# Kernel tuning notes

Hardware: AMD Instinct MI355X
Metric: run time of the kernel (lower is better)

The kernel has to match this reference:

```python
import jax, jax.numpy as jnp
import numpy as np

DIM = 64
LSH_NUM_PROJS = 7
BLOCK_SIZE = 256
SAMPLE_SIZE = 256
MIN_SEQ_LEN = 2048


def _unit_hamming(n):
    # Gray-code-like permutation used by AngularLSH so adjacent hash ids differ by 1 bit
    a = np.arange(2)
    for i in range(1, n):
        a = np.concatenate([a, a[::-1] + 2 ** i])
    return jnp.asarray(a, dtype=jnp.int32)

_PERM = _unit_hamming(LSH_NUM_PROJS)                                  # [2^P]
_ENC = (2 ** jnp.arange(LSH_NUM_PROJS)).reshape(1, 1, 1, LSH_NUM_PROJS)


def _lsh_hash(mat, proj_dir):
    # mat: [b,h,n,d], proj_dir: [1,1,d,P] -> hash ids [b,h,n]
    mask = jnp.matmul(mat, proj_dir) > 0
    bin_ids = (mask * _ENC).sum(-1)
    return _PERM[bin_ids]


def _exact_attention(q, k, v, scale, causal=False, bias=None):
    qk = jnp.einsum('bhnd,bhmd->bhnm', q, k) * scale
    if causal:
        n, m = q.shape[2], k.shape[2]
        qk = qk + jnp.triu(jnp.full((n, m), jnp.finfo(q.dtype).min, q.dtype), 1)[None, None]
    if bias is not None:
        qk = qk + bias
    lse = jax.scipy.special.logsumexp(qk, axis=-1, keepdims=True)      # [b,h,n,1]
    out = jnp.einsum('bhnm,bhmd->bhnd', jnp.exp(qk - lse), v)
    return out, lse


def _add_attn(a1, l1, a2, l2):
    c = (1.0 / (1.0 + jnp.exp(l2 - l1))).astype(a1.dtype)
    attn = c * a1 + (1 - c) * a2
    lse = l1 - jnp.log(c + jnp.finfo(l1.dtype).eps)
    return attn, lse


def _indexing(x, idx, chunk_size=-1):
    # x: [b,h,n,d], idx: [b,h,s] -> [b,h,s,d] (padded up to a multiple of chunk_size)
    g = jnp.take_along_axis(x, idx[..., None], axis=2)
    n = g.shape[2]
    if chunk_size > 0 and n % chunk_size != 0:
        pad = -n % chunk_size
        g = jnp.pad(g, ((0, 0), (0, 0), (0, pad), (0, 0)))
    return g


def _no_causal(q, k, v, scale, proj_dir, level):
    b, h, n_q, d = q.shape
    n_k = k.shape[2]
    if MIN_SEQ_LEN > n_q:
        return _exact_attention(q, k, v, scale, causal=False)
    q_idx = jnp.argsort(_lsh_hash(q, proj_dir), axis=2)
    k_idx = jnp.argsort(_lsh_hash(k, proj_dir), axis=2)
    q_idx_inv = jnp.argsort(q_idx, axis=2)
    kbs = BLOCK_SIZE
    q_s = _indexing(q, q_idx, kbs)
    k_s = _indexing(k, k_idx, kbs)
    v_s = _indexing(v, k_idx, kbs)
    num_blocks = k_s.shape[2] // kbs
    qbs = q_s.shape[2] // num_blocks
    # block-diagonal attention over LSH-sorted buckets
    q_blk = q_s.reshape(-1, 1, qbs, d)
    k_blk = k_s.reshape(-1, 1, kbs, d)
    v_blk = v_s.reshape(-1, 1, kbs, d)
    attn_block, lse_block = _exact_attention(q_blk, k_blk, v_blk, scale, causal=False)
    attn_block = attn_block.reshape(b, h, q_s.shape[2], -1)
    lse_block = lse_block.reshape(b, h, q_s.shape[2], -1)
    if q_s.shape[2] != n_q:
        attn_block = attn_block[:, :, :n_q, :]
        lse_block = lse_block[:, :, :n_q, :]
        q_s = q_s[:, :, :n_q, :]
        k_s = k_s[:, :, :n_k, :]
        v_s = v_s[:, :, :n_k, :]
    S = SAMPLE_SIZE
    if S > 0 and n_q > qbs and n_k > kbs:
        rng = jax.random.fold_in(jax.random.key(42), level)
        sampled = jax.random.randint(rng, (b, h, S), 0, n_k)
        v_sub = _indexing(v_s, sampled)
        k_sub = _indexing(k_s, sampled)
        offset = jnp.arange(n_q)[None, :, None]                         # (1,n,1)
        bm = (offset // qbs) == (sampled // kbs).reshape(-1, 1, S)      # (b*h,n,S)
        bias = bm.reshape(b, h, n_q, S).astype(q_s.dtype) * jnp.finfo(q_s.dtype).min
        attn_res, lse_res = _exact_attention(q_s, k_sub, v_sub, scale, causal=False, bias=bias)
        lse_res = lse_res + jnp.asarray(np.log(n_k / S), lse_res.dtype)
        attn, lse = _add_attn(attn_block, lse_block, attn_res, lse_res)
    else:
        attn, lse = attn_block, lse_block
    attn = _indexing(attn, q_idx_inv)
    lse = _indexing(lse, q_idx_inv)
    return attn, lse


def _hyper(q, k, v, scale, proj_dir, level=0):
    b, h, n_k, d = k.shape
    n_q = q.shape[2]
    if n_k <= MIN_SEQ_LEN:
        return _exact_attention(q, k, v, scale, causal=True)
    # recursive causal split: block-diagonal halves + un-masked lower-left quadrant
    q_bd = q.reshape(b, 2 * h, n_q // 2, d)
    k_bd = k.reshape(b, 2 * h, n_k // 2, d)
    v_bd = v.reshape(b, 2 * h, n_k // 2, d)
    attn_bd, lse_bd = _hyper(q_bd, k_bd, v_bd, scale, proj_dir, level + 1)
    attn_bd = attn_bd.reshape(b, h, -1, d)
    lse_bd = lse_bd.reshape(b, h, -1, 1)
    a_un, l_un = _no_causal(q[:, :, n_k // 2:, :], k[:, :, :n_k // 2, :],
                            v[:, :, :n_k // 2, :], scale, proj_dir, 100 + level)
    a_up, l_up = attn_bd[:, :, :n_q // 2, :], lse_bd[:, :, :n_q // 2, :]
    a_dn, l_dn = _add_attn(attn_bd[:, :, n_q // 2:, :], lse_bd[:, :, n_q // 2:, :], a_un, l_un)
    return jnp.concatenate([a_up, a_dn], axis=2), jnp.concatenate([l_up, l_dn], axis=2)


def setup_inputs() -> dict:
    rng = jax.random.key(0)
    kq, kk, kv, kp = jax.random.split(rng, 4)
    B, H, N, D = 1, 8, 8192, 64
    return {
        'query': jax.random.normal(kq, (B, H, N, D), jnp.float32),
        'key': jax.random.normal(kk, (B, H, N, D), jnp.float32),
        'value': jax.random.normal(kv, (B, H, N, D), jnp.float32),
        'proj_dir': jax.random.normal(kp, (1, 1, D, LSH_NUM_PROJS), jnp.float32),
    }


def reference(query, key, value, proj_dir):
    scale = query.shape[-1] ** -0.5
    attn, lse = _hyper(query, key, value, scale, proj_dir)
    return attn
```

## Files before the change

### kernel.cpp

```cpp
#include <hip/hip_runtime.h>
#include <stdint.h>
#include <math.h>

#define H 8
#define NSEQ 8192
#define D 64
#define SC2 0.18033688011112042f
#define LN2F 0.69314718055994531f
#define THR2 10.0f
#define EPSF 1.1920928955078125e-07f

typedef short v8s __attribute__((ext_vector_type(8)));
typedef float v4f __attribute__((ext_vector_type(4)));
typedef unsigned short ushort_t;

#define MFMA16(a,b,c) __builtin_amdgcn_mfma_f32_16x16x32_bf16((a),(b),(c),0,0,0)
#define SWZ(row, cb)    (((row)*128) + ((cb) ^ ((((row)&7))<<4)))
#define SWZ256(row, cb) (((row)*256) + ((cb) ^ ((((row)&7))<<4)))

__device__ __forceinline__ float exp2x(float x){
  float r; asm("v_exp_f32 %0, %1" : "=v"(r) : "v"(x)); return r;
}
__device__ __forceinline__ unsigned int cvtpk(float a, float b){
  unsigned int r; asm("v_cvt_pk_bf16_f32 %0, %1, %2" : "=v"(r) : "v"(a), "v"(b)); return r;
}
#define VONES (v8s){0x3F80,0x3F80,0x3F80,0x3F80,0x3F80,0x3F80,0x3F80,0x3F80}

__global__ __launch_bounds__(256) void prep_hash(
    const float* __restrict__ q, const float* __restrict__ k, const float* __restrict__ v,
    const float* __restrict__ proj,
    ushort_t* __restrict__ qb, ushort_t* __restrict__ kb, ushort_t* __restrict__ vb,
    int* __restrict__ hq, int* __restrict__ hk)
{
  __shared__ float tile[64][65];
  __shared__ float pj[448];
  __shared__ int pbuf[4][64];
  const int bid = blockIdx.x;
  const int t = threadIdx.x;
  if (bid >= 2048){
    const int tix = bid - 2048;
    size_t off = (size_t)tix*4096 + t*16;
    float4 f0 = *(const float4*)(v + off);
    float4 f1 = *(const float4*)(v + off + 4);
    float4 f2 = *(const float4*)(v + off + 8);
    float4 f3 = *(const float4*)(v + off + 12);
    uint4 o0, o1;
    o0.x = cvtpk(f0.x, f0.y);  o0.y = cvtpk(f0.z, f0.w);
    o0.z = cvtpk(f1.x, f1.y);  o0.w = cvtpk(f1.z, f1.w);
    o1.x = cvtpk(f2.x, f2.y);  o1.y = cvtpk(f2.z, f2.w);
    o1.z = cvtpk(f3.x, f3.y);  o1.w = cvtpk(f3.z, f3.w);
    *(uint4*)(vb + off) = o0;
    *(uint4*)(vb + off + 8) = o1;
    return;
  }
  const int isk = bid & 1;
  const int tix = bid >> 1;
  const int rowbase = tix << 6;
  const float* src = isk ? k : q;
  ushort_t* dstb = isk ? kb : qb;
  int* dsth = isk ? hk : hq;
  for (int i = t; i < 448; i += 256) pj[i] = proj[i];
  {
    const int r = t >> 2, cg = (t & 3) << 4;
    const float* s = src + (size_t)(rowbase + r)*64 + cg;
    float4 f0 = *(const float4*)(s);
    float4 f1 = *(const float4*)(s + 4);
    float4 f2 = *(const float4*)(s + 8);
    float4 f3 = *(const float4*)(s + 12);
    tile[r][cg+0]=f0.x;  tile[r][cg+1]=f0.y;  tile[r][cg+2]=f0.z;  tile[r][cg+3]=f0.w;
    tile[r][cg+4]=f1.x;  tile[r][cg+5]=f1.y;  tile[r][cg+6]=f1.z;  tile[r][cg+7]=f1.w;
    tile[r][cg+8]=f2.x;  tile[r][cg+9]=f2.y;  tile[r][cg+10]=f2.z; tile[r][cg+11]=f2.w;
    tile[r][cg+12]=f3.x; tile[r][cg+13]=f3.y; tile[r][cg+14]=f3.z; tile[r][cg+15]=f3.w;
    uint4 o0, o1;
    o0.x = cvtpk(f0.x, f0.y);  o0.y = cvtpk(f0.z, f0.w);
    o0.z = cvtpk(f1.x, f1.y);  o0.w = cvtpk(f1.z, f1.w);
    o1.x = cvtpk(f2.x, f2.y);  o1.y = cvtpk(f2.z, f2.w);
    o1.z = cvtpk(f3.x, f3.y);  o1.w = cvtpk(f3.z, f3.w);
    *(uint4*)(dstb + (size_t)(rowbase + r)*64 + cg) = o0;
    *(uint4*)(dstb + (size_t)(rowbase + r)*64 + cg + 8) = o1;
  }
  __syncthreads();
  {
    const int r = t & 63, pg = t >> 6;
    const int p2 = (pg < 3) ? (pg + 4) : 6;
    float d0 = 0.0f, d1 = 0.0f;
    for (int d = 0; d < 64; ++d){
      float x = tile[r][d];
      d0 = fmaf(x, pj[d*7 + pg], d0);
      d1 = fmaf(x, pj[d*7 + p2], d1);
    }
    int pb = (d0 > 0.0f ? (1 << pg) : 0);
    if (pg < 3 && d1 > 0.0f) pb |= (1 << (pg + 4));
    pbuf[pg][r] = pb;
  }
  __syncthreads();
  if (t < 64){
    int b = pbuf[0][t] | pbuf[1][t] | pbuf[2][t] | pbuf[3][t];
    dsth[rowbase + t] = b ^ (b >> 1);
  }
}

__device__ __forceinline__ void tf2x32(uint32_t k0, uint32_t k1,
                                       uint32_t x0, uint32_t x1,
                                       uint32_t& o0, uint32_t& o1)
{
  uint32_t ks0 = k0, ks1 = k1, ks2 = k0 ^ k1 ^ 0x1BD11BDAu;
  x0 += ks0; x1 += ks1;
#define RND(r) { x0 += x1; x1 = (x1 << (r)) | (x1 >> (32-(r))); x1 ^= x0; }
  RND(13) RND(15) RND(26) RND(6)  x0 += ks1; x1 += ks2 + 1u;
  RND(17) RND(29) RND(16) RND(24) x0 += ks2; x1 += ks0 + 2u;
  RND(13) RND(15) RND(26) RND(6)  x0 += ks0; x1 += ks1 + 3u;
  RND(17) RND(29) RND(16) RND(24) x0 += ks1; x1 += ks2 + 4u;
  RND(13) RND(15) RND(26) RND(6)  x0 += ks2; x1 += ks0 + 5u;
#undef RND
  o0 = x0; o1 = x1;
}

__device__ __forceinline__ void qk8(const v8s qf[2], const char* Ks, int lo, int hi, v4f sa[8]){
  __builtin_amdgcn_s_setprio(1);
#pragma unroll
  for (int st = 0; st < 8; ++st){
#pragma unroll
    for (int kc = 0; kc < 2; ++kc){
      v8s bf = *(const v8s*)(Ks + SWZ(st*16 + lo, kc*64 + hi*16));
      sa[st] = MFMA16(qf[kc], bf, sa[st]);
    }
  }
  __builtin_amdgcn_s_setprio(0);
}

__device__ __forceinline__ void sm_pv8(v4f sa[8], char* Pw, const char* VTs,
                                       int lo, int hi, float m[4], v4f o[5]){
  float tm[4];
  bool grow = false;
#pragma unroll
  for (int reg = 0; reg < 4; ++reg){
    float a = fmaxf(fmaxf(sa[0][reg], sa[1][reg]), fmaxf(sa[2][reg], sa[3][reg]));
    float b = fmaxf(fmaxf(sa[4][reg], sa[5][reg]), fmaxf(sa[6][reg], sa[7][reg]));
    tm[reg] = fmaxf(a, b);
    grow = grow || (tm[reg] > m[reg] + THR2);
  }
  if (__any(grow)){
#pragma unroll
    for (int reg = 0; reg < 4; ++reg){
      float t = tm[reg];
      t = fmaxf(t, __shfl_xor(t, 1));
      t = fmaxf(t, __shfl_xor(t, 2));
      t = fmaxf(t, __shfl_xor(t, 4));
      t = fmaxf(t, __shfl_xor(t, 8));
      float mn = fmaxf(m[reg], t);
      float corr = exp2x(m[reg] - mn);
      m[reg] = mn;
#pragma unroll
      for (int dt = 0; dt < 5; ++dt) o[dt][reg] *= corr;
    }
  }
#pragma unroll
  for (int reg = 0; reg < 4; ++reg){
    float mr = m[reg];
    uint4 pw;
    pw.x = cvtpk(exp2x(sa[0][reg]-mr), exp2x(sa[1][reg]-mr));
    pw.y = cvtpk(exp2x(sa[2][reg]-mr), exp2x(sa[3][reg]-mr));
    pw.z = cvtpk(exp2x(sa[4][reg]-mr), exp2x(sa[5][reg]-mr));
    pw.w = cvtpk(exp2x(sa[6][reg]-mr), exp2x(sa[7][reg]-mr));
    *(uint4*)(Pw + SWZ256(hi*4 + reg, 16*lo)) = pw;
  }
  asm volatile("" ::: "memory");
  __builtin_amdgcn_s_setprio(1);
#pragma unroll
  for (int kb = 0; kb < 4; ++kb){
    v8s pa = *(const v8s*)(Pw + SWZ256(lo, kb*64 + hi*16));
#pragma unroll
    for (int dt = 0; dt < 4; ++dt){
      v8s vbr = *(const v8s*)(VTs + SWZ256(dt*16 + lo, kb*64 + hi*16));
      o[dt] = MFMA16(pa, vbr, o[dt]);
    }
    o[4] = MFMA16(pa, VONES, o[4]);
  }
  __builtin_amdgcn_s_setprio(0);
}

__device__ __forceinline__ void vt_write(char* VTs, uint2 vr0, uint2 vr1, uint2 vr2, uint2 vr3,
                                         int vdg, int vlo, int vsth){
  const int cb = 16*vlo + vsth*8;
  uint2 w;
  w.x = (vr0.x & 0xFFFFu) | ((vr1.x & 0xFFFFu) << 16);
  w.y = (vr2.x & 0xFFFFu) | ((vr3.x & 0xFFFFu) << 16);
  *(uint2*)(VTs + SWZ256(vdg*4 + 0, cb)) = w;
  w.x = (vr0.x >> 16) | (vr1.x & 0xFFFF0000u);
  w.y = (vr2.x >> 16) | (vr3.x & 0xFFFF0000u);
  *(uint2*)(VTs + SWZ256(vdg*4 + 1, cb)) = w;
  w.x = (vr0.y & 0xFFFFu) | ((vr1.y & 0xFFFFu) << 16);
  w.y = (vr2.y & 0xFFFFu) | ((vr3.y & 0xFFFFu) << 16);
  *(uint2*)(VTs + SWZ256(vdg*4 + 2, cb)) = w;
  w.x = (vr0.y >> 16) | (vr1.y & 0xFFFF0000u);
  w.y = (vr2.y >> 16) | (vr3.y & 0xFFFF0000u);
  *(uint2*)(VTs + SWZ256(vdg*4 + 3, cb)) = w;
}

__global__ __launch_bounds__(512, 4) void diag_sort(
    const ushort_t* __restrict__ qb, const ushort_t* __restrict__ kb, const ushort_t* __restrict__ vb,
    float* __restrict__ out, float* __restrict__ lse,
    const int* __restrict__ hq, const int* __restrict__ hk,
    int* __restrict__ q100, int* __restrict__ k100,
    int* __restrict__ q101, int* __restrict__ k101,
    int* __restrict__ s100, int* __restrict__ s101)
{
  __shared__ __align__(16) char lds[66048];
  const int bid0 = blockIdx.x;
  const int tid = threadIdx.x;

  if (bid0 < 48){
    unsigned short (*hist)[128] = (unsigned short(*)[128])lds;
    unsigned short (*off )[128] = (unsigned short(*)[128])(lds + 32768);
    int* bstart = (int*)(lds + 65536);
    const int t = tid;
    if (t < 128){
      int gid = bid0*128 + t;
      int level, span, idx; int* outp;
      if (gid < 2048){ level = 100; span = 4096; outp = s100; idx = gid; }
      else           { level = 101; span = 2048; outp = s101; idx = gid - 2048; }
      uint32_t r0, r1; tf2x32(0u, 42u, 0u, (uint32_t)level, r0, r1);
      uint32_t k20, k21; tf2x32(r0, r1, 0u, 1u, k20, k21);
      uint32_t o0, o1; tf2x32(k20, k21, 0u, (uint32_t)idx, o0, o1);
      outp[idx] = (int)((o0 ^ o1) % (uint32_t)span);
    }
    const int* src = nullptr; int n = 0, base = 0; int* outp = nullptr;
    if (bid0 < 8)       { int h = bid0;     src = hq + h*NSEQ + 4096;        n = 4096; base = 4096;          outp = q100 + h*4096; }
    else if (bid0 < 16) { int h = bid0 - 8; src = hk + h*NSEQ;               n = 4096; base = 0;             outp = k100 + h*4096; }
    else if (bid0 < 32) { int id = bid0-16; int h = id>>1, p = id&1;
                          src = hq + h*NSEQ + p*4096 + 2048;                 n = 2048; base = p*4096 + 2048; outp = q101 + id*2048; }
    else                { int id = bid0-32; int h = id>>1, p = id&1;
                          src = hk + h*NSEQ + p*4096;                        n = 2048; base = p*4096;       outp = k101 + id*2048; }
    const int chunk = n >> 7;
    if (t < 128) for (int b = 0; b < 128; ++b) hist[t][b] = 0;
    __syncthreads();
    const int* mysrc = src + (t & 127) * chunk;
    if (t < 128) for (int i = 0; i < chunk; ++i) hist[t][mysrc[i]]++;
    __syncthreads();
    if (t < 128){
      int s = 0;
      for (int tt = 0; tt < 128; ++tt) s += hist[tt][t];
      bstart[t] = s;
    }
    __syncthreads();
    if (t == 0){
      int run = 0;
      for (int b = 0; b < 128; ++b){ int c = bstart[b]; bstart[b] = run; run += c; }
    }
    __syncthreads();
    if (t < 128){
      unsigned int run = (unsigned int)bstart[t];
      for (int tt = 0; tt < 128; ++tt){ off[tt][t] = (unsigned short)run; run += hist[tt][t]; }
    }
    __syncthreads();
    if (t < 128){
      for (int i = 0; i < chunk; ++i){
        int hsh = mysrc[i];
        unsigned short pos = off[t][hsh]++;
        outp[pos] = base + t * chunk + i;
      }
    }
    return;
  }

  char* Ks  = lds;
  char* VTs = lds + 16384;
  char* Ps  = lds + 32768;
  const int bid = bid0 - 48;
  const int xcd = bid & 7, sl = bid >> 3;
  const int inst = xcd*4 + (sl >> 4);
  const int pi = sl & 15;
  const int h = inst >> 2, tblk = inst & 3;
  const size_t hoff = (size_t)h * NSEQ * D;
  const ushort_t* qh = qb + hoff; const ushort_t* kh = kb + hoff; const ushort_t* vh = vb + hoff;
  const int blkbase = tblk * 2048;
  const int w = tid >> 6, lane = tid & 63;
  const int lo = lane & 15, hi = lane >> 4;
  char* Pw = Ps + w*4096;
  const int kr = tid >> 2, kq = tid & 3;
  const int vlo = tid & 15, vdg = (tid >> 4) & 15, vsth = tid >> 8;

  const int qt  = (w < 4) ? (31 - pi) : pi;
  const int wq  = w & 3;
  const int nkt   = (31 - pi)/2 + 1;
  const int mynkt = qt/2 + 1;
  const int qpos0 = qt*64 + wq*16;

  v8s qf[2];
  {
    const ushort_t* r = qh + (size_t)(blkbase + qpos0 + lo) * D;
    qf[0] = *(const v8s*)(r + hi*8);
    qf[1] = *(const v8s*)(r + 32 + hi*8);
  }
  const v4f vz = {0.0f, 0.0f, 0.0f, 0.0f};
  v4f o[5] = {vz, vz, vz, vz, vz};
  float m[4] = {-INFINITY, -INFINITY, -INFINITY, -INFINITY};

  uint4 kreg0, kreg1; uint2 vr0, vr1, vr2, vr3;
#define DLOAD(kt) { \
    const ushort_t* ksr = kh + (size_t)(blkbase + (kt)*128 + kr)*D + kq*16; \
    kreg0 = *(const uint4*)ksr; \
    kreg1 = *(const uint4*)(ksr + 8); \
    const ushort_t* vs = vh + (size_t)(blkbase + (kt)*128 + vsth*64 + vlo)*D + vdg*4; \
    vr0 = *(const uint2*)(vs); \
    vr1 = *(const uint2*)(vs + 16*D); \
    vr2 = *(const uint2*)(vs + 32*D); \
    vr3 = *(const uint2*)(vs + 48*D); }

  DLOAD(0);
#pragma unroll 1
  for (int kt = 0; kt < nkt; ++kt){
    *(uint4*)(Ks + SWZ(kr, kq*32))      = kreg0;
    *(uint4*)(Ks + SWZ(kr, kq*32 + 16)) = kreg1;
    vt_write(VTs, vr0, vr1, vr2, vr3, vdg, vlo, vsth);
    __syncthreads();
    if (kt + 1 < nkt) DLOAD(kt+1);
    if (kt < mynkt){
      v4f sa[8] = {vz, vz, vz, vz, vz, vz, vz, vz};
      qk8(qf, Ks, lo, hi, sa);
#pragma unroll
      for (int st = 0; st < 8; ++st) sa[st] *= SC2;
      if (kt == mynkt - 1){
#pragma unroll
        for (int st = 0; st < 8; ++st){
          int kpos = kt*128 + st*16 + lo;
#pragma unroll
          for (int reg = 0; reg < 4; ++reg)
            if (kpos > qpos0 + hi*4 + reg) sa[st][reg] = -INFINITY;
        }
      }
      sm_pv8(sa, Pw, VTs, lo, hi, m, o);
    }
    __syncthreads();
  }
#undef DLOAD
#pragma unroll
  for (int reg = 0; reg < 4; ++reg){
    int rw = blkbase + qpos0 + hi*4 + reg;
    float lsum = o[4][reg];
    float inv = 1.0f / lsum;
#pragma unroll
    for (int dt = 0; dt < 4; ++dt)
      out[hoff + (size_t)rw*D + dt*16 + lo] = o[dt][reg] * inv;
    if (lo == 0) lse[h*NSEQ + rw] = m[reg]*LN2F + logf(lsum);
  }
}

__device__ __forceinline__ int nc_key(const int* __restrict__ ki, const int* __restrict__ sp,
                                      int qblk, int kt, int pos, int& msk){
  if (kt < 2){ msk = 0; return ki[qblk*256 + kt*128 + pos]; }
  int s = sp[(kt-2)*128 + pos]; msk = ((s >> 8) == qblk) ? 1 : 0; return ki[s];
}

template<int LEVEL>
__global__ __launch_bounds__(512, 4) void nc_mfma(
    const ushort_t* __restrict__ qb, const ushort_t* __restrict__ kb, const ushort_t* __restrict__ vb,
    float* __restrict__ out, float* __restrict__ lse,
    const int* __restrict__ qidx, const int* __restrict__ kidx, const int* __restrict__ samp)
{
  __shared__ __align__(16) char Ks[16384];
  __shared__ __align__(16) char VTs[16384];
  __shared__ __align__(16) char Ps[8][4096];
  __shared__ int kmk[128];
  const int bid = blockIdx.x;
  int inst, jb;
  if (LEVEL == 101){ int xcd = bid & 7, sl = bid >> 3; inst = xcd*2 + (sl >> 4); jb = sl & 15; }
  else             { inst = bid & 7; jb = bid >> 3; }
  const float delta2 = (LEVEL == 101) ? 3.0f : 4.0f;
  const int seglen = (LEVEL == 101) ? 2048 : 4096;
  const int* qi = qidx + inst*seglen;
  const int* ki = kidx + inst*seglen;
  const int* sp = samp + inst*256;
  const int h = (LEVEL == 101) ? (inst >> 1) : inst;
  const int qblk = jb >> 1;
  const size_t hoff = (size_t)h * NSEQ * D;
  const ushort_t* qh = qb + hoff; const ushort_t* kh = kb + hoff; const ushort_t* vh = vb + hoff;
  const int tid = threadIdx.x;
  const int w = tid >> 6, lane = tid & 63;
  const int lo = lane & 15, hi = lane >> 4;
  char* Pw = Ps[w];
  const int kr = tid >> 2, kq = tid & 3;
  const int vlo = tid & 15, vdg = (tid >> 4) & 15, vsth = tid >> 8;

  int orig[4];
  v8s qf[2];
  {
    int qrl = qi[jb*128 + w*16 + lo];
    const ushort_t* r = qh + (size_t)qrl * D;
    qf[0] = *(const v8s*)(r + hi*8);
    qf[1] = *(const v8s*)(r + 32 + hi*8);
#pragma unroll
    for (int reg = 0; reg < 4; ++reg) orig[reg] = qi[jb*128 + w*16 + hi*4 + reg];
  }
  const v4f vz = {0.0f, 0.0f, 0.0f, 0.0f};
  v4f o[5] = {vz, vz, vz, vz, vz};
  float m[4] = {-INFINITY, -INFINITY, -INFINITY, -INFINITY};

  uint4 kreg0, kreg1; uint2 vr0, vr1, vr2, vr3; int msk;
#define NLOAD(kt) { \
    int krow = nc_key(ki, sp, qblk, kt, kr, msk); \
    const ushort_t* ksr = kh + (size_t)krow*D + kq*16; \
    kreg0 = *(const uint4*)ksr; \
    kreg1 = *(const uint4*)(ksr + 8); \
    int m_; \
    int g0 = nc_key(ki, sp, qblk, kt, vsth*64 + vlo,      m_); \
    int g1 = nc_key(ki, sp, qblk, kt, vsth*64 + 16 + vlo, m_); \
    int g2 = nc_key(ki, sp, qblk, kt, vsth*64 + 32 + vlo, m_); \
    int g3 = nc_key(ki, sp, qblk, kt, vsth*64 + 48 + vlo, m_); \
    vr0 = *(const uint2*)(vh + (size_t)g0*D + vdg*4); \
    vr1 = *(const uint2*)(vh + (size_t)g1*D + vdg*4); \
    vr2 = *(const uint2*)(vh + (size_t)g2*D + vdg*4); \
    vr3 = *(const uint2*)(vh + (size_t)g3*D + vdg*4); }

  NLOAD(0);
#pragma unroll 1
  for (int kt = 0; kt < 4; ++kt){
    *(uint4*)(Ks + SWZ(kr, kq*32))      = kreg0;
    *(uint4*)(Ks + SWZ(kr, kq*32 + 16)) = kreg1;
    if (kq == 0) kmk[kr] = msk;
    vt_write(VTs, vr0, vr1, vr2, vr3, vdg, vlo, vsth);
    __syncthreads();
    if (kt + 1 < 4) NLOAD(kt+1);
    v4f sa[8] = {vz, vz, vz, vz, vz, vz, vz, vz};
    qk8(qf, Ks, lo, hi, sa);
    if (kt < 2){
#pragma unroll
      for (int st = 0; st < 8; ++st) sa[st] *= SC2;
    } else {
#pragma unroll
      for (int st = 0; st < 8; ++st){
        if (kmk[st*16 + lo]) sa[st] = (v4f){-INFINITY, -INFINITY, -INFINITY, -INFINITY};
        else                 sa[st] = sa[st]*SC2 + delta2;
      }
    }
    sm_pv8(sa, Pw, VTs, lo, hi, m, o);
    __syncthreads();
  }
#undef NLOAD
#pragma unroll
  for (int reg = 0; reg < 4; ++reg){
    int og = orig[reg];
    float lsum = o[4][reg];
    float l1v = lse[h*NSEQ + og];
    float l2v = m[reg]*LN2F + logf(lsum);
    float c = 1.0f / (1.0f + __expf(l2v - l1v));
    float inv = (1.0f - c) / lsum;
#pragma unroll
    for (int dt = 0; dt < 4; ++dt){
      float* ap = out + hoff + (size_t)og*D + dt*16 + lo;
      *ap = c * (*ap) + inv * o[dt][reg];
    }
    if (lo == 0) lse[h*NSEQ + og] = l1v - logf(c + EPSF);
  }
}

extern "C" void kernel_launch(void* const* d_in, const int* in_sizes, int n_in,
                              void* d_out, int out_size, void* d_ws, size_t ws_size,
                              hipStream_t stream)
{
  const float* q    = (const float*)d_in[0];
  const float* k    = (const float*)d_in[1];
  const float* v    = (const float*)d_in[2];
  const float* proj = (const float*)d_in[3];
  float* out = (float*)d_out;

  char* ws = (char*)d_ws;
  float* lse = (float*)ws;
  int* hq   = (int*)(ws + 262144);
  int* hk   = (int*)(ws + 524288);
  int* q100 = (int*)(ws + 786432);
  int* k100 = (int*)(ws + 917504);
  int* q101 = (int*)(ws + 1048576);
  int* k101 = (int*)(ws + 1179648);
  int* s100 = (int*)(ws + 1310720);
  int* s101 = (int*)(ws + 1318912);
  ushort_t* qb = (ushort_t*)(ws + 1335296);
  ushort_t* kb = qb + (size_t)H*NSEQ*D;
  ushort_t* vb = kb + (size_t)H*NSEQ*D;

  prep_hash    <<<dim3(3072), dim3(256), 0, stream>>>(q, k, v, proj, qb, kb, vb, hq, hk);
  diag_sort    <<<dim3(560),  dim3(512), 0, stream>>>(qb, kb, vb, out, lse, hq, hk,
                                                      q100, k100, q101, k101, s100, s101);
  nc_mfma<101> <<<dim3(256),  dim3(512), 0, stream>>>(qb, kb, vb, out, lse, q101, k101, s101);
  nc_mfma<100> <<<dim3(256),  dim3(512), 0, stream>>>(qb, kb, vb, out, lse, q100, k100, s100);
}
```

Before: 113.0 us.

## Run both non-causal levels in one launch and merge level-100 results afterward

The level-101 and level-100 non-causal attention kernels are fused into a single 512-block launch so both can run concurrently instead of back-to-back. Level 100 now writes its normalized partial output as bf16 plus its LSE to a scratch buffer, and a new merge kernel combines that with the existing output. The per-wave P buffer is halved by doing the softmax/PV step in two 128-key halves, and the histogram is narrowed to bytes, cutting LDS use to raise occupancy. The trade-off is an extra kernel launch, an extra round trip through global memory, and bf16 rounding of the level-100 partial result.

```diff
diff --git a/kernel.cpp b/kernel.cpp
--- a/kernel.cpp
+++ b/kernel.cpp
@@ -23,6 +23,11 @@
 }
 __device__ __forceinline__ unsigned int cvtpk(float a, float b){
   unsigned int r; asm("v_cvt_pk_bf16_f32 %0, %1, %2" : "=v"(r) : "v"(a), "v"(b)); return r;
+}
+__device__ __forceinline__ ushort_t f2bf(float f){
+  union { float f; unsigned int u; } c; c.f = f;
+  unsigned int u = c.u + 0x7FFFu + ((c.u >> 16) & 1u);
+  return (ushort_t)(u >> 16);
 }
 #define VONES (v8s){0x3F80,0x3F80,0x3F80,0x3F80,0x3F80,0x3F80,0x3F80,0x3F80}
 
@@ -129,8 +134,8 @@
   __builtin_amdgcn_s_setprio(0);
 }
 
-__device__ __forceinline__ void sm_pv8(v4f sa[8], char* Pw, const char* VTs,
-                                       int lo, int hi, float m[4], v4f o[5]){
+__device__ __forceinline__ void sm_pv8s(v4f sa[8], char* Pw, const char* VTs,
+                                        int lo, int hi, float m[4], v4f o[5]){
   float tm[4];
   bool grow = false;
 #pragma unroll
@@ -156,33 +161,35 @@
     }
   }
 #pragma unroll
-  for (int reg = 0; reg < 4; ++reg){
-    float mr = m[reg];
-    uint4 pw;
-    pw.x = cvtpk(exp2x(sa[0][reg]-mr), exp2x(sa[1][reg]-mr));
-    pw.y = cvtpk(exp2x(sa[2][reg]-mr), exp2x(sa[3][reg]-mr));
-    pw.z = cvtpk(exp2x(sa[4][reg]-mr), exp2x(sa[5][reg]-mr));
-    pw.w = cvtpk(exp2x(sa[6][reg]-mr), exp2x(sa[7][reg]-mr));
-    *(uint4*)(Pw + SWZ256(hi*4 + reg, 16*lo)) = pw;
-  }
-  asm volatile("" ::: "memory");
-  __builtin_amdgcn_s_setprio(1);
-#pragma unroll
-  for (int kb = 0; kb < 4; ++kb){
-    v8s pa = *(const v8s*)(Pw + SWZ256(lo, kb*64 + hi*16));
-#pragma unroll
-    for (int dt = 0; dt < 4; ++dt){
-      v8s vbr = *(const v8s*)(VTs + SWZ256(dt*16 + lo, kb*64 + hi*16));
-      o[dt] = MFMA16(pa, vbr, o[dt]);
-    }
-    o[4] = MFMA16(pa, VONES, o[4]);
-  }
-  __builtin_amdgcn_s_setprio(0);
-}
-
-__device__ __forceinline__ void vt_write(char* VTs, uint2 vr0, uint2 vr1, uint2 vr2, uint2 vr3,
-                                         int vdg, int vlo, int vsth){
-  const int cb = 16*vlo + vsth*8;
+  for (int hh = 0; hh < 2; ++hh){
+#pragma unroll
+    for (int reg = 0; reg < 4; ++reg){
+      float mr = m[reg];
+      uint2 pw;
+      pw.x = cvtpk(exp2x(sa[hh*4+0][reg]-mr), exp2x(sa[hh*4+1][reg]-mr));
+      pw.y = cvtpk(exp2x(sa[hh*4+2][reg]-mr), exp2x(sa[hh*4+3][reg]-mr));
+      *(uint2*)(Pw + SWZ(hi*4 + reg, 8*lo)) = pw;
+    }
+    asm volatile("" ::: "memory");
+    __builtin_amdgcn_s_setprio(1);
+#pragma unroll
+    for (int kb = 0; kb < 2; ++kb){
+      v8s pa = *(const v8s*)(Pw + SWZ(lo, kb*64 + hi*16));
+#pragma unroll
+      for (int dt = 0; dt < 4; ++dt){
+        v8s vbr = *(const v8s*)(VTs + SWZ256(dt*16 + lo, hh*128 + kb*64 + hi*16));
+        o[dt] = MFMA16(pa, vbr, o[dt]);
+      }
+      o[4] = MFMA16(pa, VONES, o[4]);
+    }
+    __builtin_amdgcn_s_setprio(0);
+    asm volatile("" ::: "memory");
+  }
+}
+
+__device__ __forceinline__ void vt_write_h(char* VTs, uint2 vr0, uint2 vr1, uint2 vr2, uint2 vr3,
+                                           int vdg, int vlo, int vsth){
+  const int cb = vsth*128 + vlo*8;
   uint2 w;
   w.x = (vr0.x & 0xFFFFu) | ((vr1.x & 0xFFFFu) << 16);
   w.y = (vr2.x & 0xFFFFu) | ((vr3.x & 0xFFFFu) << 16);
@@ -206,14 +213,14 @@
     int* __restrict__ q101, int* __restrict__ k101,
     int* __restrict__ s100, int* __restrict__ s101)
 {
-  __shared__ __align__(16) char lds[66048];
+  __shared__ __align__(16) char lds[49664];
   const int bid0 = blockIdx.x;
   const int tid = threadIdx.x;
 
   if (bid0 < 48){
-    unsigned short (*hist)[128] = (unsigned short(*)[128])lds;
-    unsigned short (*off )[128] = (unsigned short(*)[128])(lds + 32768);
-    int* bstart = (int*)(lds + 65536);
+    unsigned char  (*hist)[128] = (unsigned char (*)[128])lds;
+    unsigned short (*off )[128] = (unsigned short(*)[128])(lds + 16384);
+    int* bstart = (int*)(lds + 49152);
     const int t = tid;
     if (t < 128){
       int gid = bid0*128 + t;
@@ -277,7 +284,7 @@
   const int blkbase = tblk * 2048;
   const int w = tid >> 6, lane = tid & 63;
   const int lo = lane & 15, hi = lane >> 4;
-  char* Pw = Ps + w*4096;
+  char* Pw = Ps + w*2048;
   const int kr = tid >> 2, kq = tid & 3;
   const int vlo = tid & 15, vdg = (tid >> 4) & 15, vsth = tid >> 8;
 
@@ -313,7 +320,7 @@
   for (int kt = 0; kt < nkt; ++kt){
     *(uint4*)(Ks + SWZ(kr, kq*32))      = kreg0;
     *(uint4*)(Ks + SWZ(kr, kq*32 + 16)) = kreg1;
-    vt_write(VTs, vr0, vr1, vr2, vr3, vdg, vlo, vsth);
+    vt_write_h(VTs, vr0, vr1, vr2, vr3, vdg, vlo, vsth);
     __syncthreads();
     if (kt + 1 < nkt) DLOAD(kt+1);
     if (kt < mynkt){
@@ -330,7 +337,7 @@
             if (kpos > qpos0 + hi*4 + reg) sa[st][reg] = -INFINITY;
         }
       }
-      sm_pv8(sa, Pw, VTs, lo, hi, m, o);
+      sm_pv8s(sa, Pw, VTs, lo, hi, m, o);
     }
     __syncthreads();
   }
@@ -353,26 +360,31 @@
   int s = sp[(kt-2)*128 + pos]; msk = ((s >> 8) == qblk) ? 1 : 0; return ki[s];
 }
 
-template<int LEVEL>
-__global__ __launch_bounds__(512, 4) void nc_mfma(
+__global__ __launch_bounds__(512, 4) void nc_both(
     const ushort_t* __restrict__ qb, const ushort_t* __restrict__ kb, const ushort_t* __restrict__ vb,
     float* __restrict__ out, float* __restrict__ lse,
-    const int* __restrict__ qidx, const int* __restrict__ kidx, const int* __restrict__ samp)
+    const int* __restrict__ q101, const int* __restrict__ k101, const int* __restrict__ s101,
+    const int* __restrict__ q100, const int* __restrict__ k100, const int* __restrict__ s100,
+    ushort_t* __restrict__ a100, float* __restrict__ lse100)
 {
   __shared__ __align__(16) char Ks[16384];
   __shared__ __align__(16) char VTs[16384];
-  __shared__ __align__(16) char Ps[8][4096];
+  __shared__ __align__(16) char Ps[8][2048];
   __shared__ int kmk[128];
   const int bid = blockIdx.x;
-  int inst, jb;
-  if (LEVEL == 101){ int xcd = bid & 7, sl = bid >> 3; inst = xcd*2 + (sl >> 4); jb = sl & 15; }
-  else             { inst = bid & 7; jb = bid >> 3; }
-  const float delta2 = (LEVEL == 101) ? 3.0f : 4.0f;
-  const int seglen = (LEVEL == 101) ? 2048 : 4096;
-  const int* qi = qidx + inst*seglen;
-  const int* ki = kidx + inst*seglen;
-  const int* sp = samp + inst*256;
-  const int h = (LEVEL == 101) ? (inst >> 1) : inst;
+  const bool lvl101 = bid < 256;
+  int inst, jb; float delta2; int seglen;
+  const int *qi, *ki, *sp;
+  if (lvl101){
+    int xcd = bid & 7, sl = bid >> 3; inst = xcd*2 + (sl >> 4); jb = sl & 15;
+    delta2 = 3.0f; seglen = 2048;
+    qi = q101 + inst*seglen; ki = k101 + inst*seglen; sp = s101 + inst*256;
+  } else {
+    int b2 = bid - 256; inst = b2 & 7; jb = b2 >> 3;
+    delta2 = 4.0f; seglen = 4096;
+    qi = q100 + inst*seglen; ki = k100 + inst*seglen; sp = s100 + inst*256;
+  }
+  const int h = lvl101 ? (inst >> 1) : inst;
   const int qblk = jb >> 1;
   const size_t hoff = (size_t)h * NSEQ * D;
   const ushort_t* qh = qb + hoff; const ushort_t* kh = kb + hoff; const ushort_t* vh = vb + hoff;
@@ -419,7 +431,7 @@
     *(uint4*)(Ks + SWZ(kr, kq*32))      = kreg0;
     *(uint4*)(Ks + SWZ(kr, kq*32 + 16)) = kreg1;
     if (kq == 0) kmk[kr] = msk;
-    vt_write(VTs, vr0, vr1, vr2, vr3, vdg, vlo, vsth);
+    vt_write_h(VTs, vr0, vr1, vr2, vr3, vdg, vlo, vsth);
     __syncthreads();
     if (kt + 1 < 4) NLOAD(kt+1);
     v4f sa[8] = {vz, vz, vz, vz, vz, vz, vz, vz};
@@ -434,25 +446,67 @@
         else                 sa[st] = sa[st]*SC2 + delta2;
       }
     }
-    sm_pv8(sa, Pw, VTs, lo, hi, m, o);
+    sm_pv8s(sa, Pw, VTs, lo, hi, m, o);
     __syncthreads();
   }
 #undef NLOAD
-#pragma unroll
-  for (int reg = 0; reg < 4; ++reg){
-    int og = orig[reg];
-    float lsum = o[4][reg];
-    float l1v = lse[h*NSEQ + og];
-    float l2v = m[reg]*LN2F + logf(lsum);
-    float c = 1.0f / (1.0f + __expf(l2v - l1v));
-    float inv = (1.0f - c) / lsum;
-#pragma unroll
-    for (int dt = 0; dt < 4; ++dt){
-      float* ap = out + hoff + (size_t)og*D + dt*16 + lo;
-      *ap = c * (*ap) + inv * o[dt][reg];
-    }
-    if (lo == 0) lse[h*NSEQ + og] = l1v - logf(c + EPSF);
-  }
+  if (lvl101){
+#pragma unroll
+    for (int reg = 0; reg < 4; ++reg){
+      int og = orig[reg];
+      float lsum = o[4][reg];
+      float l1v = lse[h*NSEQ + og];
+      float l2v = m[reg]*LN2F + logf(lsum);
+      float c = 1.0f / (1.0f + __expf(l2v - l1v));
+      float inv = (1.0f - c) / lsum;
+#pragma unroll
+      for (int dt = 0; dt < 4; ++dt){
+        float* ap = out + hoff + (size_t)og*D + dt*16 + lo;
+        *ap = c * (*ap) + inv * o[dt][reg];
+      }
+      if (lo == 0) lse[h*NSEQ + og] = l1v - logf(c + EPSF);
+    }
+  } else {
+#pragma unroll
+    for (int reg = 0; reg < 4; ++reg){
+      int og = orig[reg];
+      float lsum = o[4][reg];
+      float inv = 1.0f / lsum;
+      ushort_t* arow = a100 + ((size_t)h*NSEQ + og)*D;
+#pragma unroll
+      for (int dt = 0; dt < 4; ++dt)
+        arow[dt*16 + lo] = f2bf(o[dt][reg] * inv);
+      if (lo == 0) lse100[h*NSEQ + og] = m[reg]*LN2F + logf(lsum);
+    }
+  }
+}
+
+__global__ __launch_bounds__(256) void merge_kernel(
+    float* __restrict__ out, const float* __restrict__ lse,
+    const ushort_t* __restrict__ a100, const float* __restrict__ lse100)
+{
+  const int gid = blockIdx.x * 256 + threadIdx.x;
+  const size_t e = (size_t)gid * 4;
+  const int h = (int)(e >> 18);
+  const int rem = (int)(e & 262143);
+  const int og = 4096 + (rem >> 6);
+  const size_t row = (size_t)h*NSEQ + og;
+  const float l1 = lse[row];
+  const float l2 = lse100[row];
+  const float c = 1.0f / (1.0f + __expf(l2 - l1));
+  const float ic = 1.0f - c;
+  float* op = out + ((size_t)h*NSEQ*D) + (size_t)og*D + (rem & 63);
+  float4 ov = *(float4*)op;
+  uint2 av = *(const uint2*)(a100 + row*D + (rem & 63));
+  float a0 = __uint_as_float((av.x & 0xFFFFu) << 16);
+  float a1 = __uint_as_float((av.x & 0xFFFF0000u));
+  float a2 = __uint_as_float((av.y & 0xFFFFu) << 16);
+  float a3 = __uint_as_float((av.y & 0xFFFF0000u));
+  ov.x = c*ov.x + ic*a0;
+  ov.y = c*ov.y + ic*a1;
+  ov.z = c*ov.z + ic*a2;
+  ov.w = c*ov.w + ic*a3;
+  *(float4*)op = ov;
 }
 
 extern "C" void kernel_launch(void* const* d_in, const int* in_sizes, int n_in,
@@ -478,10 +532,14 @@
   ushort_t* qb = (ushort_t*)(ws + 1335296);
   ushort_t* kb = qb + (size_t)H*NSEQ*D;
   ushort_t* vb = kb + (size_t)H*NSEQ*D;
+  ushort_t* a100 = vb + (size_t)H*NSEQ*D;
+  float* lse100 = (float*)(a100 + (size_t)H*NSEQ*D);
 
   prep_hash    <<<dim3(3072), dim3(256), 0, stream>>>(q, k, v, proj, qb, kb, vb, hq, hk);
   diag_sort    <<<dim3(560),  dim3(512), 0, stream>>>(qb, kb, vb, out, lse, hq, hk,
                                                       q100, k100, q101, k101, s100, s101);
-  nc_mfma<101> <<<dim3(256),  dim3(512), 0, stream>>>(qb, kb, vb, out, lse, q101, k101, s101);
-  nc_mfma<100> <<<dim3(256),  dim3(512), 0, stream>>>(qb, kb, vb, out, lse, q100, k100, s100);
-}
+  nc_both      <<<dim3(512),  dim3(512), 0, stream>>>(qb, kb, vb, out, lse,
+                                                      q101, k101, s101, q100, k100, s100,
+                                                      a100, lse100);
+  merge_kernel <<<dim3(2048), dim3(256), 0, stream>>>(out, lse, a100, lse100);
+}
```

New measurement: 107.4 us. 4.9% less time.
